# Optimization experiments

Measured on AMD Instinct MI355X. Metric: run time of the kernel, lower is better.

The kernel has to match this reference:

```python
import jax, jax.numpy as jnp
import numpy as np

D_HEAD = 64

def setup_inputs() -> dict:
    key = jax.random.key(0)
    kq, kk, kv, kc = jax.random.split(key, 4)
    B, H, T, D = 2, 16, 2048, D_HEAD
    Q = jax.random.normal(kq, (B, H, T, D), dtype=jnp.float32)
    K = jax.random.normal(kk, (B, H, T, D), dtype=jnp.float32)
    V = jax.random.normal(kv, (B, H, T, D), dtype=jnp.float32)
    # causal mask: True = attend
    mask = jnp.tril(jnp.ones((T, T), dtype=jnp.bool_))
    curvature = jax.random.normal(kc, (H, D, D), dtype=jnp.float32) * 0.02
    return {"Q": Q, "K": K, "V": V, "mask": mask, "curvature": curvature}

def reference(Q, K, V, mask, curvature):
    scale = 1.0 / np.sqrt(Q.shape[-1]).astype(np.float32)
    # per-head learned rotation of Q
    Q_rot = jnp.einsum('bhtd,hde->bhte', Q, curvature)
    scores = jnp.einsum('bhtd,bhsd->bhts', Q_rot, K) * scale  # [B,H,T,T]
    scores = jnp.where(mask[None, None, :, :], scores, -jnp.inf)
    attn = jax.nn.softmax(scores, axis=-1)
    out = jnp.einsum('bhts,bhsd->bhtd', attn, V)
    return out
```

## Files before the change

kernel.cpp:

```cpp
#include <hip/hip_runtime.h>


typedef __attribute__((ext_vector_type(8))) short short8;
typedef __attribute__((ext_vector_type(8))) unsigned short ushort8;
typedef __attribute__((ext_vector_type(4))) float f32x4;
typedef __attribute__((ext_vector_type(2))) _Float16 half2v;
typedef __attribute__((ext_vector_type(4))) _Float16 half4;
typedef __attribute__((ext_vector_type(8))) _Float16 half8;

constexpr int Tc = 2048;
constexpr int Dc = 64;
constexpr size_t REGION = (size_t)32 * Tc * Dc;

__device__ inline unsigned short f2bf(float f) {
    union { float f; unsigned u; } x; x.f = f;
    return (unsigned short)((x.u + 0x7fffu + ((x.u >> 16) & 1u)) >> 16);
}

__device__ inline half2v pkrtz(float a, float b) {
    return __builtin_bit_cast(half2v, __builtin_amdgcn_cvt_pkrtz(a, b));
}

#define MFMA_BF16_K32(a, b, c) __builtin_amdgcn_mfma_f32_16x16x32_bf16((a), (b), (c), 0, 0, 0)
#define MFMA_F16_K16(a, b, c)  __builtin_amdgcn_mfma_f32_16x16x16f16((a), (b), (c), 0, 0, 0)

typedef __attribute__((address_space(3))) unsigned int        lds_u32;
typedef const __attribute__((address_space(1))) unsigned int  glob_u32;
__device__ __attribute__((always_inline)) inline void gl_lds16(const void* g, void* l) {
    __builtin_amdgcn_global_load_lds((glob_u32*)g, (lds_u32*)l, 16, 0, 0);
}

__global__ __launch_bounds__(256, 1)
void holo_cfrag(const float* __restrict__ Cp, unsigned short* __restrict__ cfrag_g)
{
    const int t = threadIdx.x, lane = t & 63, eb = t >> 6;
    const int l15 = lane & 15, quad = lane >> 4;
    const int h = blockIdx.x;
    const float* Cg = Cp + (size_t)h * Dc * Dc;
    #pragma unroll
    for (int half = 0; half < 2; ++half) {
        short8 b;
        #pragma unroll
        for (int jj = 0; jj < 8; ++jj) {
            const int d = half * 32 + quad * 8 + jj;
            b[jj] = (short)f2bf(Cg[d * Dc + eb * 16 + l15]);
        }
        *(short8*)(&cfrag_g[(((size_t)h * 4 + eb) * 2 + half) * 512 + lane * 8]) = b;
    }
}

__global__ __launch_bounds__(256, 4)
void holo_prep8(const float* __restrict__ Qp, const float* __restrict__ Kp,
                const float* __restrict__ Vp,
                const unsigned short* __restrict__ cfrag_g,
                unsigned short* __restrict__ qfrag_g,
                unsigned short* __restrict__ kfrag_g,
                _Float16* __restrict__ vfrag_g)
{
    __shared__ unsigned short kt[64 * 72];
    __shared__ unsigned short qt[64 * 72];
    __shared__ _Float16      vt[64 * 72];
    __shared__ unsigned short pf[64 * 72];

    const int t = threadIdx.x, lane = t & 63, w = t >> 6;
    const int l15 = lane & 15, quad = lane >> 4, wb = w * 16;
    const int n = blockIdx.x, bh = n >> 5, st = n & 31, h = bh & 15;
    const int s0 = st * 64;

    const float* Qg = Qp + ((size_t)bh * Tc + s0) * Dc;
    const float* Kg = Kp + ((size_t)bh * Tc + s0) * Dc;
    const float* Vg = Vp + ((size_t)bh * Tc + s0) * Dc;

    #pragma unroll
    for (int kk = 0; kk < 4; ++kk) {
        const int flat = kk * 1024 + t * 4;
        const int r = flat >> 6, d0 = flat & 63;
        float4 kv = *(const float4*)(&Kg[flat]);
        ushort4 kp; kp.x = f2bf(kv.x); kp.y = f2bf(kv.y); kp.z = f2bf(kv.z); kp.w = f2bf(kv.w);
        *(ushort4*)(&kt[r * 72 + d0]) = kp;
        float4 qv = *(const float4*)(&Qg[flat]);
        ushort4 qp; qp.x = f2bf(qv.x); qp.y = f2bf(qv.y); qp.z = f2bf(qv.z); qp.w = f2bf(qv.w);
        *(ushort4*)(&qt[r * 72 + d0]) = qp;
        float4 vv = *(const float4*)(&Vg[flat]);
        half4 vp;
        vp[0] = (_Float16)vv.x; vp[1] = (_Float16)vv.y;
        vp[2] = (_Float16)vv.z; vp[3] = (_Float16)vv.w;
        *(half4*)(&vt[r * 72 + d0]) = vp;
    }
    __syncthreads();

    {
        const int row = wb + l15;
        ushort8 p0 = *(const ushort8*)(&kt[row * 72 + quad * 8]);
        ushort8 p1 = *(const ushort8*)(&kt[row * 72 + 32 + quad * 8]);
        unsigned short* ktile = kfrag_g + (size_t)(bh * 32 + st) * 4096;
        *(ushort8*)(&ktile[(w * 64 + lane) * 8])        = p0;
        *(ushort8*)(&ktile[2048 + (w * 64 + lane) * 8]) = p1;
    }

    {
        half8 v0, v1;
        #pragma unroll
        for (int dn = 0; dn < 2; ++dn)
            #pragma unroll
            for (int i = 0; i < 4; ++i)
                v0[dn * 4 + i] = vt[(wb + quad * 4 + i) * 72 + dn * 16 + l15];
        #pragma unroll
        for (int dn = 0; dn < 2; ++dn)
            #pragma unroll
            for (int i = 0; i < 4; ++i)
                v1[dn * 4 + i] = vt[(wb + quad * 4 + i) * 72 + (dn + 2) * 16 + l15];
        _Float16* vtile = vfrag_g + (size_t)(bh * 32 + st) * 4096;
        *(half8*)(&vtile[(w * 64 + lane) * 8])        = v0;
        *(half8*)(&vtile[2048 + (w * 64 + lane) * 8]) = v1;
    }

    {
        short8 a0 = *(const short8*)(&qt[(wb + l15) * 72 + quad * 8]);
        short8 a1 = *(const short8*)(&qt[(wb + l15) * 72 + 32 + quad * 8]);
        #pragma unroll
        for (int eb = 0; eb < 4; ++eb) {
            short8 b0 = *(const short8*)(&cfrag_g[(((size_t)h * 4 + eb) * 2 + 0) * 512 + lane * 8]);
            short8 b1 = *(const short8*)(&cfrag_g[(((size_t)h * 4 + eb) * 2 + 1) * 512 + lane * 8]);
            f32x4 c = {0.f, 0.f, 0.f, 0.f};
            c = MFMA_BF16_K32(a0, b0, c);
            c = MFMA_BF16_K32(a1, b1, c);
            #pragma unroll
            for (int i = 0; i < 4; ++i)
                pf[(wb + quad * 4 + i) * 72 + eb * 16 + l15] = f2bf(c[i] * 0.18033688f);
        }
        __threadfence_block();
        short8 fa0 = *(const short8*)(&pf[(wb + l15) * 72 + quad * 8]);
        short8 fa1 = *(const short8*)(&pf[(wb + l15) * 72 + 32 + quad * 8]);
        const size_t strip = (size_t)bh * 128 + st * 4 + w;
        *(short8*)(&qfrag_g[strip * 1024 + lane * 8]) = fa0;
        *(short8*)(&qfrag_g[strip * 1024 + 512 + lane * 8]) = fa1;
    }
}

__global__ __launch_bounds__(256, 2)
void holo_attn15(const unsigned short* __restrict__ qfrag_g,
                 const unsigned short* __restrict__ kfrag_g,
                 const _Float16* __restrict__ vfrag_g,
                 float* __restrict__ Op)
{
    __shared__ unsigned short bufK[2][4096];
    __shared__ _Float16      bufV[2][4096];

    const int t = threadIdx.x, lane = t & 63, wid = t >> 6;
    const int l15 = lane & 15, quad = lane >> 4;

    const int id = blockIdx.x;
    const int xcd = id & 7, seq = id >> 3;
    const int u = seq & 15, v = (seq >> 4) & 1, w5 = (seq >> 5) & 1;
    const int bh = xcd * 4 + v * 2 + w5;
    const int p  = w5 ? u : 15 - u;
    const int jmax  = 2 * p + 1;
    const int jdiag = 2 * p + (wid >> 1);

    const char* kbase = (const char*)(kfrag_g + (size_t)bh * 32 * 4096);
    const char* vbase = (const char*)(vfrag_g + (size_t)bh * 32 * 4096);

    gl_lds16(kbase + wid * 1024 + lane * 16,        &bufK[0][wid * 512]);
    gl_lds16(kbase + 4096 + wid * 1024 + lane * 16, &bufK[0][2048 + wid * 512]);
    gl_lds16(vbase + wid * 1024 + lane * 16,        &bufV[0][wid * 512]);
    gl_lds16(vbase + 4096 + wid * 1024 + lane * 16, &bufV[0][2048 + wid * 512]);

    short8 qa0[2], qa1[2];
    #pragma unroll
    for (int s2 = 0; s2 < 2; ++s2) {
        const size_t strip = (size_t)bh * 128 + p * 8 + wid * 2 + s2;
        qa0[s2] = *(const short8*)(&qfrag_g[strip * 1024 + lane * 8]);
        qa1[s2] = *(const short8*)(&qfrag_g[strip * 1024 + 512 + lane * 8]);
    }

    f32x4 o[2][4];
    #pragma unroll
    for (int s2 = 0; s2 < 2; ++s2)
        #pragma unroll
        for (int dn = 0; dn < 4; ++dn) o[s2][dn] = f32x4{0.f, 0.f, 0.f, 0.f};
    float l2[2] = {0.f, 0.f};

    const int rowgA = p * 128 + wid * 32 + l15;
    const int rowgB = rowgA + 16;

    asm volatile("s_waitcnt vmcnt(0)" ::: "memory");
    __builtin_amdgcn_sched_barrier(0);
    __syncthreads();

    int cur = 0;
    for (int j = 0; j <= jmax; ++j) {
        if (j < jmax) {
            const char* ks = kbase + (size_t)(j + 1) * 8192;
            const char* vs = vbase + (size_t)(j + 1) * 8192;
            const int nb = cur ^ 1;
            gl_lds16(ks + wid * 1024 + lane * 16,        &bufK[nb][wid * 512]);
            gl_lds16(ks + 4096 + wid * 1024 + lane * 16, &bufK[nb][2048 + wid * 512]);
            gl_lds16(vs + wid * 1024 + lane * 16,        &bufV[nb][wid * 512]);
            gl_lds16(vs + 4096 + wid * 1024 + lane * 16, &bufV[nb][2048 + wid * 512]);
        }

        if (j <= jdiag) {
            const unsigned short* Kl = &bufK[cur][0];
            const _Float16*       Vl = &bufV[cur][0];

            f32x4 stA[4], stB[4];
            __builtin_amdgcn_s_setprio(1);
            #pragma unroll
            for (int tn = 0; tn < 4; ++tn) {
                short8 k0 = *(const short8*)(&Kl[(tn * 64 + lane) * 8]);
                short8 k1 = *(const short8*)(&Kl[2048 + (tn * 64 + lane) * 8]);
                f32x4 cA = {0.f, 0.f, 0.f, 0.f};
                cA = MFMA_BF16_K32(k0, qa0[0], cA);
                cA = MFMA_BF16_K32(k1, qa1[0], cA);
                stA[tn] = cA;
                f32x4 cB = {0.f, 0.f, 0.f, 0.f};
                cB = MFMA_BF16_K32(k0, qa0[1], cB);
                cB = MFMA_BF16_K32(k1, qa1[1], cB);
                stB[tn] = cB;
            }
            __builtin_amdgcn_s_setprio(0);

            half4 paA[4], paB[4];
            #pragma unroll
            for (int tn = 0; tn < 4; ++tn) {
                float pA[4];
                #pragma unroll
                for (int i = 0; i < 4; ++i) {
                    float sv = stA[tn][i];
                    if (j == jdiag) {
                        const int colg = j * 64 + tn * 16 + quad * 4 + i;
                        if (colg > rowgA) sv = -1e30f;
                    }
                    pA[i] = __builtin_amdgcn_exp2f(sv);
                    l2[0] += pA[i];
                }
                half2v lo = pkrtz(pA[0], pA[1]), hi = pkrtz(pA[2], pA[3]);
                paA[tn] = __builtin_shufflevector(lo, hi, 0, 1, 2, 3);
            }
            #pragma unroll
            for (int tn = 0; tn < 4; ++tn) {
                float pB[4];
                #pragma unroll
                for (int i = 0; i < 4; ++i) {
                    float sv = stB[tn][i];
                    if (j == jdiag) {
                        const int colg = j * 64 + tn * 16 + quad * 4 + i;
                        if (colg > rowgB) sv = -1e30f;
                    }
                    pB[i] = __builtin_amdgcn_exp2f(sv);
                    l2[1] += pB[i];
                }
                half2v lo = pkrtz(pB[0], pB[1]), hi = pkrtz(pB[2], pB[3]);
                paB[tn] = __builtin_shufflevector(lo, hi, 0, 1, 2, 3);
            }

            __builtin_amdgcn_s_setprio(1);
            #pragma unroll
            for (int tn = 0; tn < 4; ++tn) {
                half8 vl = *(const half8*)(&Vl[(tn * 64 + lane) * 8]);
                half8 vh = *(const half8*)(&Vl[2048 + (tn * 64 + lane) * 8]);
                half4 vf0 = __builtin_shufflevector(vl, vl, 0, 1, 2, 3);
                half4 vf1 = __builtin_shufflevector(vl, vl, 4, 5, 6, 7);
                half4 vf2 = __builtin_shufflevector(vh, vh, 0, 1, 2, 3);
                half4 vf3 = __builtin_shufflevector(vh, vh, 4, 5, 6, 7);
                o[0][0] = MFMA_F16_K16(vf0, paA[tn], o[0][0]);
                o[0][1] = MFMA_F16_K16(vf1, paA[tn], o[0][1]);
                o[0][2] = MFMA_F16_K16(vf2, paA[tn], o[0][2]);
                o[0][3] = MFMA_F16_K16(vf3, paA[tn], o[0][3]);
                o[1][0] = MFMA_F16_K16(vf0, paB[tn], o[1][0]);
                o[1][1] = MFMA_F16_K16(vf1, paB[tn], o[1][1]);
                o[1][2] = MFMA_F16_K16(vf2, paB[tn], o[1][2]);
                o[1][3] = MFMA_F16_K16(vf3, paB[tn], o[1][3]);
            }
            __builtin_amdgcn_s_setprio(0);
        }

        asm volatile("s_waitcnt vmcnt(0)" ::: "memory");
        __builtin_amdgcn_sched_barrier(0);
        __syncthreads();
        cur ^= 1;
    }

    #pragma unroll
    for (int s2 = 0; s2 < 2; ++s2) {
        float l = l2[s2];
        l += __shfl_xor(l, 16);
        l += __shfl_xor(l, 32);
        const float inv = 1.0f / l;
        const int rowg = rowgA + s2 * 16;
        float* dst = Op + ((size_t)bh * Tc + rowg) * Dc;
        #pragma unroll
        for (int dn = 0; dn < 4; ++dn) {
            float4 r;
            r.x = o[s2][dn][0] * inv; r.y = o[s2][dn][1] * inv;
            r.z = o[s2][dn][2] * inv; r.w = o[s2][dn][3] * inv;
            *(float4*)(&dst[dn * 16 + quad * 4]) = r;
        }
    }
}

extern "C" void kernel_launch(void* const* d_in, const int* in_sizes, int n_in,
                              void* d_out, int out_size, void* d_ws, size_t ws_size,
                              hipStream_t stream) {
    const float* Q = (const float*)d_in[0];
    const float* K = (const float*)d_in[1];
    const float* V = (const float*)d_in[2];
    const float* C = (const float*)d_in[4];
    float* O = (float*)d_out;

    unsigned short* qfrag_w = (unsigned short*)d_ws;
    unsigned short* kfrag_w = qfrag_w + REGION;
    _Float16*       vfrag_w = (_Float16*)(kfrag_w + REGION);
    unsigned short* cfrag_w = (unsigned short*)(vfrag_w + REGION);

    holo_cfrag<<<dim3(16), dim3(256), 0, stream>>>(C, cfrag_w);
    holo_prep8<<<dim3(1024), dim3(256), 0, stream>>>(Q, K, V, cfrag_w, qfrag_w, kfrag_w, vfrag_w);
    holo_attn15<<<dim3(512), dim3(256), 0, stream>>>(qfrag_w, kfrag_w, vfrag_w, O);
}
```

Baseline: 157.8 us.

## Split attention blocks to 64-row query tiles with 2 waves each

Restructures the attention kernel from 256-thread blocks covering 128 query rows to 128-thread blocks covering 64 query rows, doubling the grid to 1024 blocks. Each wave now processes only K/V tiles up to its own diagonal without idle diagonal iterations, and each wave loads twice as many K/V segments into LDS. The block-to-tile mapping is changed to balance causal work across XCDs. The aim is better load balance and less wasted diagonal work, at the cost of K/V tiles being loaded from global memory twice as often per query row.

```diff
diff --git a/kernel.cpp b/kernel.cpp
--- a/kernel.cpp
+++ b/kernel.cpp
@@ -138,8 +138,8 @@
     }
 }
 
-__global__ __launch_bounds__(256, 2)
-void holo_attn15(const unsigned short* __restrict__ qfrag_g,
+__global__ __launch_bounds__(128, 2)
+void holo_attn16(const unsigned short* __restrict__ qfrag_g,
                  const unsigned short* __restrict__ kfrag_g,
                  const _Float16* __restrict__ vfrag_g,
                  float* __restrict__ Op)
@@ -151,25 +151,28 @@
     const int l15 = lane & 15, quad = lane >> 4;
 
     const int id = blockIdx.x;
-    const int xcd = id & 7, seq = id >> 3;
-    const int u = seq & 15, v = (seq >> 4) & 1, w5 = (seq >> 5) & 1;
-    const int bh = xcd * 4 + v * 2 + w5;
-    const int p  = w5 ? u : 15 - u;
-    const int jmax  = 2 * p + 1;
-    const int jdiag = 2 * p + (wid >> 1);
+    const int xcd = id & 7, m = (id >> 3) & 31, k = id >> 8;
+    const int bh = xcd * 4 + k;
+    const int mm = (k >= 2) ? ((m + 16) & 31) : m;
+    const int qi = (k & 1) ? (31 - mm) : mm;
+    const int q0 = qi * 64;
 
     const char* kbase = (const char*)(kfrag_g + (size_t)bh * 32 * 4096);
     const char* vbase = (const char*)(vfrag_g + (size_t)bh * 32 * 4096);
 
-    gl_lds16(kbase + wid * 1024 + lane * 16,        &bufK[0][wid * 512]);
-    gl_lds16(kbase + 4096 + wid * 1024 + lane * 16, &bufK[0][2048 + wid * 512]);
-    gl_lds16(vbase + wid * 1024 + lane * 16,        &bufV[0][wid * 512]);
-    gl_lds16(vbase + 4096 + wid * 1024 + lane * 16, &bufV[0][2048 + wid * 512]);
+    #pragma unroll
+    for (int s = 0; s < 2; ++s) {
+        const int seg = wid * 2 + s;
+        gl_lds16(kbase + seg * 1024 + lane * 16,        &bufK[0][seg * 512]);
+        gl_lds16(kbase + 4096 + seg * 1024 + lane * 16, &bufK[0][2048 + seg * 512]);
+        gl_lds16(vbase + seg * 1024 + lane * 16,        &bufV[0][seg * 512]);
+        gl_lds16(vbase + 4096 + seg * 1024 + lane * 16, &bufV[0][2048 + seg * 512]);
+    }
 
     short8 qa0[2], qa1[2];
     #pragma unroll
     for (int s2 = 0; s2 < 2; ++s2) {
-        const size_t strip = (size_t)bh * 128 + p * 8 + wid * 2 + s2;
+        const size_t strip = (size_t)bh * 128 + qi * 4 + wid * 2 + s2;
         qa0[s2] = *(const short8*)(&qfrag_g[strip * 1024 + lane * 8]);
         qa1[s2] = *(const short8*)(&qfrag_g[strip * 1024 + 512 + lane * 8]);
     }
@@ -181,7 +184,7 @@
         for (int dn = 0; dn < 4; ++dn) o[s2][dn] = f32x4{0.f, 0.f, 0.f, 0.f};
     float l2[2] = {0.f, 0.f};
 
-    const int rowgA = p * 128 + wid * 32 + l15;
+    const int rowgA = q0 + wid * 32 + l15;
     const int rowgB = rowgA + 16;
 
     asm volatile("s_waitcnt vmcnt(0)" ::: "memory");
@@ -189,92 +192,94 @@
     __syncthreads();
 
     int cur = 0;
-    for (int j = 0; j <= jmax; ++j) {
-        if (j < jmax) {
+    for (int j = 0; j <= qi; ++j) {
+        if (j < qi) {
             const char* ks = kbase + (size_t)(j + 1) * 8192;
             const char* vs = vbase + (size_t)(j + 1) * 8192;
             const int nb = cur ^ 1;
-            gl_lds16(ks + wid * 1024 + lane * 16,        &bufK[nb][wid * 512]);
-            gl_lds16(ks + 4096 + wid * 1024 + lane * 16, &bufK[nb][2048 + wid * 512]);
-            gl_lds16(vs + wid * 1024 + lane * 16,        &bufV[nb][wid * 512]);
-            gl_lds16(vs + 4096 + wid * 1024 + lane * 16, &bufV[nb][2048 + wid * 512]);
-        }
-
-        if (j <= jdiag) {
-            const unsigned short* Kl = &bufK[cur][0];
-            const _Float16*       Vl = &bufV[cur][0];
-
-            f32x4 stA[4], stB[4];
-            __builtin_amdgcn_s_setprio(1);
-            #pragma unroll
-            for (int tn = 0; tn < 4; ++tn) {
-                short8 k0 = *(const short8*)(&Kl[(tn * 64 + lane) * 8]);
-                short8 k1 = *(const short8*)(&Kl[2048 + (tn * 64 + lane) * 8]);
-                f32x4 cA = {0.f, 0.f, 0.f, 0.f};
-                cA = MFMA_BF16_K32(k0, qa0[0], cA);
-                cA = MFMA_BF16_K32(k1, qa1[0], cA);
-                stA[tn] = cA;
-                f32x4 cB = {0.f, 0.f, 0.f, 0.f};
-                cB = MFMA_BF16_K32(k0, qa0[1], cB);
-                cB = MFMA_BF16_K32(k1, qa1[1], cB);
-                stB[tn] = cB;
+            #pragma unroll
+            for (int s = 0; s < 2; ++s) {
+                const int seg = wid * 2 + s;
+                gl_lds16(ks + seg * 1024 + lane * 16,        &bufK[nb][seg * 512]);
+                gl_lds16(ks + 4096 + seg * 1024 + lane * 16, &bufK[nb][2048 + seg * 512]);
+                gl_lds16(vs + seg * 1024 + lane * 16,        &bufV[nb][seg * 512]);
+                gl_lds16(vs + 4096 + seg * 1024 + lane * 16, &bufV[nb][2048 + seg * 512]);
             }
-            __builtin_amdgcn_s_setprio(0);
-
-            half4 paA[4], paB[4];
-            #pragma unroll
-            for (int tn = 0; tn < 4; ++tn) {
-                float pA[4];
-                #pragma unroll
-                for (int i = 0; i < 4; ++i) {
-                    float sv = stA[tn][i];
-                    if (j == jdiag) {
-                        const int colg = j * 64 + tn * 16 + quad * 4 + i;
-                        if (colg > rowgA) sv = -1e30f;
-                    }
-                    pA[i] = __builtin_amdgcn_exp2f(sv);
-                    l2[0] += pA[i];
+        }
+
+        const unsigned short* Kl = &bufK[cur][0];
+        const _Float16*       Vl = &bufV[cur][0];
+
+        f32x4 stA[4], stB[4];
+        __builtin_amdgcn_s_setprio(1);
+        #pragma unroll
+        for (int tn = 0; tn < 4; ++tn) {
+            short8 k0 = *(const short8*)(&Kl[(tn * 64 + lane) * 8]);
+            short8 k1 = *(const short8*)(&Kl[2048 + (tn * 64 + lane) * 8]);
+            f32x4 cA = {0.f, 0.f, 0.f, 0.f};
+            cA = MFMA_BF16_K32(k0, qa0[0], cA);
+            cA = MFMA_BF16_K32(k1, qa1[0], cA);
+            stA[tn] = cA;
+            f32x4 cB = {0.f, 0.f, 0.f, 0.f};
+            cB = MFMA_BF16_K32(k0, qa0[1], cB);
+            cB = MFMA_BF16_K32(k1, qa1[1], cB);
+            stB[tn] = cB;
+        }
+        __builtin_amdgcn_s_setprio(0);
+
+        half4 paA[4], paB[4];
+        #pragma unroll
+        for (int tn = 0; tn < 4; ++tn) {
+            float pA[4];
+            #pragma unroll
+            for (int i = 0; i < 4; ++i) {
+                float sv = stA[tn][i];
+                if (j == qi) {
+                    const int colg = j * 64 + tn * 16 + quad * 4 + i;
+                    if (colg > rowgA) sv = -1e30f;
                 }
-                half2v lo = pkrtz(pA[0], pA[1]), hi = pkrtz(pA[2], pA[3]);
-                paA[tn] = __builtin_shufflevector(lo, hi, 0, 1, 2, 3);
+                pA[i] = __builtin_amdgcn_exp2f(sv);
+                l2[0] += pA[i];
             }
-            #pragma unroll
-            for (int tn = 0; tn < 4; ++tn) {
-                float pB[4];
-                #pragma unroll
-                for (int i = 0; i < 4; ++i) {
-                    float sv = stB[tn][i];
-                    if (j == jdiag) {
-                        const int colg = j * 64 + tn * 16 + quad * 4 + i;
-                        if (colg > rowgB) sv = -1e30f;
-                    }
-                    pB[i] = __builtin_amdgcn_exp2f(sv);
-                    l2[1] += pB[i];
+            half2v lo = pkrtz(pA[0], pA[1]), hi = pkrtz(pA[2], pA[3]);
+            paA[tn] = __builtin_shufflevector(lo, hi, 0, 1, 2, 3);
+        }
+        #pragma unroll
+        for (int tn = 0; tn < 4; ++tn) {
+            float pB[4];
+            #pragma unroll
+            for (int i = 0; i < 4; ++i) {
+                float sv = stB[tn][i];
+                if (j == qi) {
+                    const int colg = j * 64 + tn * 16 + quad * 4 + i;
+                    if (colg > rowgB) sv = -1e30f;
                 }
-                half2v lo = pkrtz(pB[0], pB[1]), hi = pkrtz(pB[2], pB[3]);
-                paB[tn] = __builtin_shufflevector(lo, hi, 0, 1, 2, 3);
+                pB[i] = __builtin_amdgcn_exp2f(sv);
+                l2[1] += pB[i];
             }
-
-            __builtin_amdgcn_s_setprio(1);
-            #pragma unroll
-            for (int tn = 0; tn < 4; ++tn) {
-                half8 vl = *(const half8*)(&Vl[(tn * 64 + lane) * 8]);
-                half8 vh = *(const half8*)(&Vl[2048 + (tn * 64 + lane) * 8]);
-                half4 vf0 = __builtin_shufflevector(vl, vl, 0, 1, 2, 3);
-                half4 vf1 = __builtin_shufflevector(vl, vl, 4, 5, 6, 7);
-                half4 vf2 = __builtin_shufflevector(vh, vh, 0, 1, 2, 3);
-                half4 vf3 = __builtin_shufflevector(vh, vh, 4, 5, 6, 7);
-                o[0][0] = MFMA_F16_K16(vf0, paA[tn], o[0][0]);
-                o[0][1] = MFMA_F16_K16(vf1, paA[tn], o[0][1]);
-                o[0][2] = MFMA_F16_K16(vf2, paA[tn], o[0][2]);
-                o[0][3] = MFMA_F16_K16(vf3, paA[tn], o[0][3]);
-                o[1][0] = MFMA_F16_K16(vf0, paB[tn], o[1][0]);
-                o[1][1] = MFMA_F16_K16(vf1, paB[tn], o[1][1]);
-                o[1][2] = MFMA_F16_K16(vf2, paB[tn], o[1][2]);
-                o[1][3] = MFMA_F16_K16(vf3, paB[tn], o[1][3]);
-            }
-            __builtin_amdgcn_s_setprio(0);
-        }
+            half2v lo = pkrtz(pB[0], pB[1]), hi = pkrtz(pB[2], pB[3]);
+            paB[tn] = __builtin_shufflevector(lo, hi, 0, 1, 2, 3);
+        }
+
+        __builtin_amdgcn_s_setprio(1);
+        #pragma unroll
+        for (int tn = 0; tn < 4; ++tn) {
+            half8 vl = *(const half8*)(&Vl[(tn * 64 + lane) * 8]);
+            half8 vh = *(const half8*)(&Vl[2048 + (tn * 64 + lane) * 8]);
+            half4 vf0 = __builtin_shufflevector(vl, vl, 0, 1, 2, 3);
+            half4 vf1 = __builtin_shufflevector(vl, vl, 4, 5, 6, 7);
+            half4 vf2 = __builtin_shufflevector(vh, vh, 0, 1, 2, 3);
+            half4 vf3 = __builtin_shufflevector(vh, vh, 4, 5, 6, 7);
+            o[0][0] = MFMA_F16_K16(vf0, paA[tn], o[0][0]);
+            o[0][1] = MFMA_F16_K16(vf1, paA[tn], o[0][1]);
+            o[0][2] = MFMA_F16_K16(vf2, paA[tn], o[0][2]);
+            o[0][3] = MFMA_F16_K16(vf3, paA[tn], o[0][3]);
+            o[1][0] = MFMA_F16_K16(vf0, paB[tn], o[1][0]);
+            o[1][1] = MFMA_F16_K16(vf1, paB[tn], o[1][1]);
+            o[1][2] = MFMA_F16_K16(vf2, paB[tn], o[1][2]);
+            o[1][3] = MFMA_F16_K16(vf3, paB[tn], o[1][3]);
+        }
+        __builtin_amdgcn_s_setprio(0);
 
         asm volatile("s_waitcnt vmcnt(0)" ::: "memory");
         __builtin_amdgcn_sched_barrier(0);
@@ -316,5 +321,5 @@
 
     holo_cfrag<<<dim3(16), dim3(256), 0, stream>>>(C, cfrag_w);
     holo_prep8<<<dim3(1024), dim3(256), 0, stream>>>(Q, K, V, cfrag_w, qfrag_w, kfrag_w, vfrag_w);
-    holo_attn15<<<dim3(512), dim3(256), 0, stream>>>(qfrag_w, kfrag_w, vfrag_w, O);
-}
+    holo_attn16<<<dim3(1024), dim3(128), 0, stream>>>(qfrag_w, kfrag_w, vfrag_w, O);
+}
```

New measurement: 148.5 us. 1.06x faster.

## Split long causal query blocks across KV chunks with a separate combine kernel

Applied to the files above, without the earlier changes.

Splits each query block's KV range into chunks of up to 8 tiles, so long causal rows are processed by several workgroups (1280 blocks instead of 512). Blocks that cover a whole row write the normalized output directly. The others write unnormalized partial outputs and row sums to workspace, and a new combine kernel sums and normalizes them. Occupancy hint rises to 4 blocks per CU. This relies on the partials sharing a fixed softmax max (no running max), and it adds an extra launch plus partial-buffer traffic.

```diff
diff --git a/kernel.cpp b/kernel.cpp
--- a/kernel.cpp
+++ b/kernel.cpp
@@ -138,10 +138,12 @@
     }
 }
 
-__global__ __launch_bounds__(256, 2)
-void holo_attn15(const unsigned short* __restrict__ qfrag_g,
+__global__ __launch_bounds__(256, 4)
+void holo_attn17(const unsigned short* __restrict__ qfrag_g,
                  const unsigned short* __restrict__ kfrag_g,
                  const _Float16* __restrict__ vfrag_g,
+                 float* __restrict__ opart_g,
+                 float* __restrict__ lpart_g,
                  float* __restrict__ Op)
 {
     __shared__ unsigned short bufK[2][4096];
@@ -151,20 +153,29 @@
     const int l15 = lane & 15, quad = lane >> 4;
 
     const int id = blockIdx.x;
-    const int xcd = id & 7, seq = id >> 3;
-    const int u = seq & 15, v = (seq >> 4) & 1, w5 = (seq >> 5) & 1;
-    const int bh = xcd * 4 + v * 2 + w5;
-    const int p  = w5 ? u : 15 - u;
-    const int jmax  = 2 * p + 1;
+    const int xcd = id & 7, s = id >> 3;
+    const int bh = xcd * 4 + (s & 3);
+    int rem = s >> 2;
+    int p = 0;
+    while (true) { const int nc = (2 * p + 9) >> 3; if (rem < nc) break; rem -= nc; ++p; }
+    const int c = rem;
+    const int nch = (2 * p + 9) >> 3;
+    const int j0 = c * 8;
+    const int jlim = 2 * p + 2;
+    const int j1 = (j0 + 8 < jlim) ? j0 + 8 : jlim;
     const int jdiag = 2 * p + (wid >> 1);
 
     const char* kbase = (const char*)(kfrag_g + (size_t)bh * 32 * 4096);
     const char* vbase = (const char*)(vfrag_g + (size_t)bh * 32 * 4096);
 
-    gl_lds16(kbase + wid * 1024 + lane * 16,        &bufK[0][wid * 512]);
-    gl_lds16(kbase + 4096 + wid * 1024 + lane * 16, &bufK[0][2048 + wid * 512]);
-    gl_lds16(vbase + wid * 1024 + lane * 16,        &bufV[0][wid * 512]);
-    gl_lds16(vbase + 4096 + wid * 1024 + lane * 16, &bufV[0][2048 + wid * 512]);
+    {
+        const char* ks = kbase + (size_t)j0 * 8192;
+        const char* vs = vbase + (size_t)j0 * 8192;
+        gl_lds16(ks + wid * 1024 + lane * 16,        &bufK[0][wid * 512]);
+        gl_lds16(ks + 4096 + wid * 1024 + lane * 16, &bufK[0][2048 + wid * 512]);
+        gl_lds16(vs + wid * 1024 + lane * 16,        &bufV[0][wid * 512]);
+        gl_lds16(vs + 4096 + wid * 1024 + lane * 16, &bufV[0][2048 + wid * 512]);
+    }
 
     short8 qa0[2], qa1[2];
     #pragma unroll
@@ -189,8 +200,8 @@
     __syncthreads();
 
     int cur = 0;
-    for (int j = 0; j <= jmax; ++j) {
-        if (j < jmax) {
+    for (int j = j0; j < j1; ++j) {
+        if (j + 1 < j1) {
             const char* ks = kbase + (size_t)(j + 1) * 8192;
             const char* vs = vbase + (size_t)(j + 1) * 8192;
             const int nb = cur ^ 1;
@@ -284,19 +295,80 @@
 
     #pragma unroll
     for (int s2 = 0; s2 < 2; ++s2) {
-        float l = l2[s2];
-        l += __shfl_xor(l, 16);
-        l += __shfl_xor(l, 32);
-        const float inv = 1.0f / l;
-        const int rowg = rowgA + s2 * 16;
-        float* dst = Op + ((size_t)bh * Tc + rowg) * Dc;
-        #pragma unroll
-        for (int dn = 0; dn < 4; ++dn) {
-            float4 r;
-            r.x = o[s2][dn][0] * inv; r.y = o[s2][dn][1] * inv;
-            r.z = o[s2][dn][2] * inv; r.w = o[s2][dn][3] * inv;
-            *(float4*)(&dst[dn * 16 + quad * 4]) = r;
-        }
+        l2[s2] += __shfl_xor(l2[s2], 16);
+        l2[s2] += __shfl_xor(l2[s2], 32);
+    }
+
+    if (nch == 1) {
+        #pragma unroll
+        for (int s2 = 0; s2 < 2; ++s2) {
+            const float inv = 1.0f / l2[s2];
+            const int rowg = rowgA + s2 * 16;
+            float* dst = Op + ((size_t)bh * Tc + rowg) * Dc;
+            #pragma unroll
+            for (int dn = 0; dn < 4; ++dn) {
+                float4 r;
+                r.x = o[s2][dn][0] * inv; r.y = o[s2][dn][1] * inv;
+                r.z = o[s2][dn][2] * inv; r.w = o[s2][dn][3] * inv;
+                *(float4*)(&dst[dn * 16 + quad * 4]) = r;
+            }
+        }
+    } else {
+        const size_t slot = (size_t)(bh * 16 + p) * 4 + c;
+        #pragma unroll
+        for (int s2 = 0; s2 < 2; ++s2) {
+            const int prow = wid * 32 + s2 * 16 + l15;
+            float* od = opart_g + slot * 8192 + (size_t)prow * 64;
+            #pragma unroll
+            for (int dn = 0; dn < 4; ++dn) {
+                float4 r;
+                r.x = o[s2][dn][0]; r.y = o[s2][dn][1];
+                r.z = o[s2][dn][2]; r.w = o[s2][dn][3];
+                *(float4*)(&od[dn * 16 + quad * 4]) = r;
+            }
+            if (quad == 0) lpart_g[slot * 128 + prow] = l2[s2];
+        }
+    }
+}
+
+__global__ __launch_bounds__(256, 4)
+void holo_comb(const float* __restrict__ opart_g,
+               const float* __restrict__ lpart_g,
+               float* __restrict__ Op)
+{
+    const int u2 = blockIdx.x;
+    const int bh = u2 / 12, p = 4 + (u2 % 12);
+    const int nch = (2 * p + 9) >> 3;
+    const size_t ubase = (size_t)(bh * 16 + p) * 4;
+
+    const int t = threadIdx.x;
+    const int r = t >> 1, c0 = (t & 1) * 32;
+
+    float acc[32];
+    #pragma unroll
+    for (int k = 0; k < 32; ++k) acc[k] = 0.f;
+    float lsum = 0.f;
+
+    for (int c = 0; c < nch; ++c) {
+        const size_t slot = ubase + c;
+        lsum += lpart_g[slot * 128 + r];
+        const float* src = opart_g + slot * 8192 + (size_t)r * 64 + c0;
+        #pragma unroll
+        for (int k4 = 0; k4 < 8; ++k4) {
+            float4 v = *(const float4*)(&src[k4 * 4]);
+            acc[k4 * 4 + 0] += v.x; acc[k4 * 4 + 1] += v.y;
+            acc[k4 * 4 + 2] += v.z; acc[k4 * 4 + 3] += v.w;
+        }
+    }
+
+    const float inv = 1.0f / lsum;
+    float* dst = Op + ((size_t)bh * Tc + p * 128 + r) * Dc + c0;
+    #pragma unroll
+    for (int k4 = 0; k4 < 8; ++k4) {
+        float4 v;
+        v.x = acc[k4 * 4 + 0] * inv; v.y = acc[k4 * 4 + 1] * inv;
+        v.z = acc[k4 * 4 + 2] * inv; v.w = acc[k4 * 4 + 3] * inv;
+        *(float4*)(&dst[k4 * 4]) = v;
     }
 }
 
@@ -313,8 +385,11 @@
     unsigned short* kfrag_w = qfrag_w + REGION;
     _Float16*       vfrag_w = (_Float16*)(kfrag_w + REGION);
     unsigned short* cfrag_w = (unsigned short*)(vfrag_w + REGION);
+    float* opart_w = (float*)((char*)d_ws + ((size_t)25 << 20));
+    float* lpart_w = (float*)((char*)d_ws + ((size_t)90 << 20));
 
     holo_cfrag<<<dim3(16), dim3(256), 0, stream>>>(C, cfrag_w);
     holo_prep8<<<dim3(1024), dim3(256), 0, stream>>>(Q, K, V, cfrag_w, qfrag_w, kfrag_w, vfrag_w);
-    holo_attn15<<<dim3(512), dim3(256), 0, stream>>>(qfrag_w, kfrag_w, vfrag_w, O);
-}
+    holo_attn17<<<dim3(1280), dim3(256), 0, stream>>>(qfrag_w, kfrag_w, vfrag_w, opart_w, lpart_w, O);
+    holo_comb<<<dim3(384), dim3(256), 0, stream>>>(opart_w, lpart_w, O);
+}
```

Result: no change. 156.2 us (-1.0%).

## Split KV blocks across wave pairs per 64-row query tile and reduce via LDS

Applied to the files above, without the earlier changes.

Each workgroup now handles a 64-row query tile instead of 128 rows, and the grid doubles to 1024 blocks, scheduled longest tile first. The two wave pairs take alternating KV blocks (even and odd), and their partial outputs and row sums are combined through LDS at the end. This removes the per-wave causal imbalance, where some waves idled past the diagonal. The launch bound rises to 4 blocks per CU and LDS is reused for the reduction. In exchange it adds an extra sync and reduction, reloads K/V per smaller tile (more global traffic), and puts more pressure on registers.

```diff
diff --git a/kernel.cpp b/kernel.cpp
--- a/kernel.cpp
+++ b/kernel.cpp
@@ -138,25 +138,28 @@
     }
 }
 
-__global__ __launch_bounds__(256, 2)
-void holo_attn15(const unsigned short* __restrict__ qfrag_g,
+__global__ __launch_bounds__(256, 4)
+void holo_attn20(const unsigned short* __restrict__ qfrag_g,
                  const unsigned short* __restrict__ kfrag_g,
                  const _Float16* __restrict__ vfrag_g,
                  float* __restrict__ Op)
 {
-    __shared__ unsigned short bufK[2][4096];
-    __shared__ _Float16      bufV[2][4096];
+    __shared__ __align__(16) unsigned char smem[32768];
+    unsigned short (*bufK)[4096] = (unsigned short (*)[4096])smem;
+    _Float16       (*bufV)[4096] = (_Float16 (*)[4096])(smem + 16384);
+    float* lds_o = (float*)smem;
+    float* lds_l = (float*)(smem + 24576);
 
     const int t = threadIdx.x, lane = t & 63, wid = t >> 6;
     const int l15 = lane & 15, quad = lane >> 4;
+    const int hv  = wid & 1;
+    const int par = wid >> 1;
 
     const int id = blockIdx.x;
-    const int xcd = id & 7, seq = id >> 3;
-    const int u = seq & 15, v = (seq >> 4) & 1, w5 = (seq >> 5) & 1;
-    const int bh = xcd * 4 + v * 2 + w5;
-    const int p  = w5 ? u : 15 - u;
-    const int jmax  = 2 * p + 1;
-    const int jdiag = 2 * p + (wid >> 1);
+    const int xcd = id & 7, sseq = id >> 3;
+    const int qi = 31 - (sseq >> 2);
+    const int bh = xcd * 4 + (sseq & 3);
+    const int q0 = qi * 64;
 
     const char* kbase = (const char*)(kfrag_g + (size_t)bh * 32 * 4096);
     const char* vbase = (const char*)(vfrag_g + (size_t)bh * 32 * 4096);
@@ -169,7 +172,7 @@
     short8 qa0[2], qa1[2];
     #pragma unroll
     for (int s2 = 0; s2 < 2; ++s2) {
-        const size_t strip = (size_t)bh * 128 + p * 8 + wid * 2 + s2;
+        const size_t strip = (size_t)bh * 128 + qi * 4 + (2 * hv + s2);
         qa0[s2] = *(const short8*)(&qfrag_g[strip * 1024 + lane * 8]);
         qa1[s2] = *(const short8*)(&qfrag_g[strip * 1024 + 512 + lane * 8]);
     }
@@ -181,7 +184,7 @@
         for (int dn = 0; dn < 4; ++dn) o[s2][dn] = f32x4{0.f, 0.f, 0.f, 0.f};
     float l2[2] = {0.f, 0.f};
 
-    const int rowgA = p * 128 + wid * 32 + l15;
+    const int rowgA = q0 + (2 * hv) * 16 + l15;
     const int rowgB = rowgA + 16;
 
     asm volatile("s_waitcnt vmcnt(0)" ::: "memory");
@@ -189,8 +192,8 @@
     __syncthreads();
 
     int cur = 0;
-    for (int j = 0; j <= jmax; ++j) {
-        if (j < jmax) {
+    for (int j = 0; j <= qi; ++j) {
+        if (j < qi) {
             const char* ks = kbase + (size_t)(j + 1) * 8192;
             const char* vs = vbase + (size_t)(j + 1) * 8192;
             const int nb = cur ^ 1;
@@ -200,7 +203,7 @@
             gl_lds16(vs + 4096 + wid * 1024 + lane * 16, &bufV[nb][2048 + wid * 512]);
         }
 
-        if (j <= jdiag) {
+        if ((j & 1) == par) {
             const unsigned short* Kl = &bufK[cur][0];
             const _Float16*       Vl = &bufV[cur][0];
 
@@ -224,35 +227,24 @@
             half4 paA[4], paB[4];
             #pragma unroll
             for (int tn = 0; tn < 4; ++tn) {
-                float pA[4];
+                float pA[4], pB[4];
                 #pragma unroll
                 for (int i = 0; i < 4; ++i) {
-                    float sv = stA[tn][i];
-                    if (j == jdiag) {
+                    float svA = stA[tn][i], svB = stB[tn][i];
+                    if (j == qi) {
                         const int colg = j * 64 + tn * 16 + quad * 4 + i;
-                        if (colg > rowgA) sv = -1e30f;
+                        if (colg > rowgA) svA = -1e30f;
+                        if (colg > rowgB) svB = -1e30f;
                     }
-                    pA[i] = __builtin_amdgcn_exp2f(sv);
+                    pA[i] = __builtin_amdgcn_exp2f(svA);
+                    pB[i] = __builtin_amdgcn_exp2f(svB);
                     l2[0] += pA[i];
-                }
-                half2v lo = pkrtz(pA[0], pA[1]), hi = pkrtz(pA[2], pA[3]);
-                paA[tn] = __builtin_shufflevector(lo, hi, 0, 1, 2, 3);
-            }
-            #pragma unroll
-            for (int tn = 0; tn < 4; ++tn) {
-                float pB[4];
-                #pragma unroll
-                for (int i = 0; i < 4; ++i) {
-                    float sv = stB[tn][i];
-                    if (j == jdiag) {
-                        const int colg = j * 64 + tn * 16 + quad * 4 + i;
-                        if (colg > rowgB) sv = -1e30f;
-                    }
-                    pB[i] = __builtin_amdgcn_exp2f(sv);
                     l2[1] += pB[i];
                 }
-                half2v lo = pkrtz(pB[0], pB[1]), hi = pkrtz(pB[2], pB[3]);
-                paB[tn] = __builtin_shufflevector(lo, hi, 0, 1, 2, 3);
+                half2v loA = pkrtz(pA[0], pA[1]), hiA = pkrtz(pA[2], pA[3]);
+                paA[tn] = __builtin_shufflevector(loA, hiA, 0, 1, 2, 3);
+                half2v loB = pkrtz(pB[0], pB[1]), hiB = pkrtz(pB[2], pB[3]);
+                paB[tn] = __builtin_shufflevector(loB, hiB, 0, 1, 2, 3);
             }
 
             __builtin_amdgcn_s_setprio(1);
@@ -284,18 +276,41 @@
 
     #pragma unroll
     for (int s2 = 0; s2 < 2; ++s2) {
-        float l = l2[s2];
-        l += __shfl_xor(l, 16);
-        l += __shfl_xor(l, 32);
-        const float inv = 1.0f / l;
-        const int rowg = rowgA + s2 * 16;
-        float* dst = Op + ((size_t)bh * Tc + rowg) * Dc;
-        #pragma unroll
-        for (int dn = 0; dn < 4; ++dn) {
-            float4 r;
-            r.x = o[s2][dn][0] * inv; r.y = o[s2][dn][1] * inv;
-            r.z = o[s2][dn][2] * inv; r.w = o[s2][dn][3] * inv;
-            *(float4*)(&dst[dn * 16 + quad * 4]) = r;
+        l2[s2] += __shfl_xor(l2[s2], 16);
+        l2[s2] += __shfl_xor(l2[s2], 32);
+    }
+
+    if (par == 1) {
+        #pragma unroll
+        for (int s2 = 0; s2 < 2; ++s2) {
+            float* po = lds_o + (size_t)((hv * 2 + s2) * 16 + l15) * 68;
+            #pragma unroll
+            for (int dn = 0; dn < 4; ++dn) {
+                float4 r;
+                r.x = o[s2][dn][0]; r.y = o[s2][dn][1];
+                r.z = o[s2][dn][2]; r.w = o[s2][dn][3];
+                *(float4*)(&po[dn * 16 + quad * 4]) = r;
+            }
+            if (quad == 0) lds_l[(hv * 2 + s2) * 16 + l15] = l2[s2];
+        }
+    }
+    __syncthreads();
+    if (par == 0) {
+        #pragma unroll
+        for (int s2 = 0; s2 < 2; ++s2) {
+            const float inv = 1.0f / (l2[s2] + lds_l[(hv * 2 + s2) * 16 + l15]);
+            const int rowg = q0 + (2 * hv + s2) * 16 + l15;
+            float* dst = Op + ((size_t)bh * Tc + rowg) * Dc;
+            const float* po = lds_o + (size_t)((hv * 2 + s2) * 16 + l15) * 68;
+            #pragma unroll
+            for (int dn = 0; dn < 4; ++dn) {
+                float4 r;
+                r.x = (o[s2][dn][0] + po[dn * 16 + quad * 4 + 0]) * inv;
+                r.y = (o[s2][dn][1] + po[dn * 16 + quad * 4 + 1]) * inv;
+                r.z = (o[s2][dn][2] + po[dn * 16 + quad * 4 + 2]) * inv;
+                r.w = (o[s2][dn][3] + po[dn * 16 + quad * 4 + 3]) * inv;
+                *(float4*)(&dst[dn * 16 + quad * 4]) = r;
+            }
         }
     }
 }
@@ -316,5 +331,5 @@
 
     holo_cfrag<<<dim3(16), dim3(256), 0, stream>>>(C, cfrag_w);
     holo_prep8<<<dim3(1024), dim3(256), 0, stream>>>(Q, K, V, cfrag_w, qfrag_w, kfrag_w, vfrag_w);
-    holo_attn15<<<dim3(512), dim3(256), 0, stream>>>(qfrag_w, kfrag_w, vfrag_w, O);
-}
+    holo_attn20<<<dim3(1024), dim3(256), 0, stream>>>(qfrag_w, kfrag_w, vfrag_w, O);
+}
```

Result: faster. 140.3 us (-11.1%).
